# Kernel tuning notes

Measured on AMD Instinct MI355X. Metric: run time of the kernel, lower is better.

Reference implementation:

```python
import jax, jax.numpy as jnp
import numpy as np

# JAX reference for BERN-NN-Implicit LayerModule.forward.
# Semantics: for each output node i,
#   combined_over[i]  = sum_j relu(W)[i,j]*inputs_over[j] + (-relu(-W))[i,j]*inputs_under[j] + bias[i]
#   combined_under[i] = sum_j (-relu(-W))[i,j]*inputs_over[j] + relu(W)[i,j]*inputs_under[j] + bias[i]
# With all input Bernstein polynomials at equal degree, SumModule reduces to addition
# and prod_input_weights reduces to a weighted sum over the previous-layer neuron axis.

N_IN = 64      # previous-layer neurons
SIZE = 64      # nodes in this layer
G = 513        # Bernstein coefficient grid per dim (degree 512 + 1), dims = 2


def setup_inputs() -> dict:
    key = jax.random.key(0)
    k1, k2, k3, k4 = jax.random.split(key, 4)
    return {
        "inputs_under": jax.random.normal(k1, (N_IN, G, G), dtype=jnp.float32),
        "inputs_over": jax.random.normal(k2, (N_IN, G, G), dtype=jnp.float32),
        "weights": jax.random.normal(k3, (SIZE, N_IN), dtype=jnp.float32),
        "biases": jax.random.normal(k4, (SIZE,), dtype=jnp.float32),
        "layer_idx": 0,
    }


def reference(inputs_under, inputs_over, weights, biases, layer_idx):
    w_pos = jax.nn.relu(weights)          # [size, n_in]
    w_neg = -jax.nn.relu(-weights)        # [size, n_in]
    b = biases[:, None, None]             # [size, 1, 1]
    # [size, G, G] Bernstein coefficient grids per output node
    combined_over = (jnp.einsum("oi,ixy->oxy", w_pos, inputs_over)
                     + jnp.einsum("oi,ixy->oxy", w_neg, inputs_under)) + b
    combined_under = (jnp.einsum("oi,ixy->oxy", w_neg, inputs_over)
                      + jnp.einsum("oi,ixy->oxy", w_pos, inputs_under)) + b
    return combined_under, combined_over
```

## Files before the change

### kernel.cpp

```cpp
#include <hip/hip_runtime.h>

constexpr int PIX   = 513 * 513;
constexpr int NTILE = 128;

typedef short bf16x8 __attribute__((ext_vector_type(8)));
typedef float f32x4  __attribute__((ext_vector_type(4)));

__device__ __forceinline__ unsigned short f2bf(float f) {
    unsigned u = __builtin_bit_cast(unsigned, f);
    u += 0x7fffu + ((u >> 16) & 1u);
    return (unsigned short)(u >> 16);
}

__global__ __launch_bounds__(256, 2) void mfma_bounds_kernel(
    const float* __restrict__ under,
    const float* __restrict__ over,
    const float* __restrict__ W,
    const float* __restrict__ bias,
    float* __restrict__ out_under,
    float* __restrict__ out_over)
{
    __shared__ alignas(16) unsigned short Wl[128 * 128];
    __shared__ alignas(16) unsigned short Xt[NTILE * 128];
    __shared__ float Bl[64];

    const int t = threadIdx.x;
    const int pxbase = blockIdx.x * NTILE;

    if (pxbase + NTILE > PIX) {
        if (t < 128) {
            const int m = t;
            const int o = m & 63;
            const float* prim = (m < 64) ? over  : under;
            const float* sec  = (m < 64) ? under : over;
            for (int p = pxbase; p < PIX; ++p) {
                float acc = bias[o];
                for (int i = 0; i < 64; ++i) {
                    const float w = W[o * 64 + i];
                    acc += fmaxf(w, 0.f) * prim[(size_t)i * PIX + p]
                         + fminf(w, 0.f) * sec [(size_t)i * PIX + p];
                }
                if (m < 64) out_over [(size_t)m        * PIX + p] = acc;
                else        out_under[(size_t)(m - 64) * PIX + p] = acc;
            }
        }
        return;
    }

    #pragma unroll 4
    for (int e = 0; e < 32; ++e) {
        const int pidx = t + 256 * e;
        const int r  = pidx >> 6;
        const int c0 = (pidx & 63) * 2;
        const float w0 = W[(r & 63) * 64 + (c0 & 63)];
        const float w1 = W[(r & 63) * 64 + ((c0 + 1) & 63)];
        const bool same = ((c0 < 64) == (r < 64));
        const float v0 = same ? fmaxf(w0, 0.f) : fminf(w0, 0.f);
        const float v1 = same ? fmaxf(w1, 0.f) : fminf(w1, 0.f);
        const unsigned pack = (unsigned)f2bf(v0) | ((unsigned)f2bf(v1) << 16);
        const int off = r * 256 + ((c0 * 2) ^ ((r & 7) << 4));
        *(unsigned*)((char*)Wl + off) = pack;
    }
    if (t < 64) Bl[t] = bias[t];

    {
        const int px    = t & 127;
        const int khalf = t >> 7;
        const float* src = khalf ? under : over;
        const size_t p = (size_t)pxbase + px;
        #pragma unroll 8
        for (int j = 0; j < 32; ++j) {
            const int row = 2 * j;
            const float x0 = src[(size_t)row       * PIX + p];
            const float x1 = src[(size_t)(row + 1) * PIX + p];
            const unsigned pack = (unsigned)f2bf(x0) | ((unsigned)f2bf(x1) << 16);
            const int kbyte = 4 * j + 128 * khalf;
            const int off = px * 256 + (kbyte ^ ((px & 7) << 4));
            *(unsigned*)((char*)Xt + off) = pack;
        }
    }
    __syncthreads();

    const int wv   = t >> 6;
    const int lane = t & 63;
    const int lrow = lane & 15;
    const int lg   = lane >> 4;
    const int m0   = wv * 32;

    float bf[2][4];
    #pragma unroll
    for (int mt = 0; mt < 2; ++mt)
        #pragma unroll
        for (int r = 0; r < 4; ++r)
            bf[mt][r] = Bl[(m0 + mt * 16 + lg * 4 + r) & 63];

    bf16x8 A[2][4];
    #pragma unroll
    for (int mt = 0; mt < 2; ++mt)
        #pragma unroll
        for (int ks = 0; ks < 4; ++ks) {
            const int row = m0 + mt * 16 + lrow;
            const int ch  = ks * 4 + lg;
            A[mt][ks] = *(const bf16x8*)((const char*)Wl +
                          row * 256 + ((ch * 16) ^ ((row & 7) << 4)));
        }

    f32x4 acc[2][8];
    #pragma unroll
    for (int mt = 0; mt < 2; ++mt)
        #pragma unroll
        for (int nt = 0; nt < 8; ++nt) {
            f32x4 v = {bf[mt][0], bf[mt][1], bf[mt][2], bf[mt][3]};
            acc[mt][nt] = v;
        }

    #pragma unroll
    for (int nt = 0; nt < 8; ++nt) {
        bf16x8 Bf[4];
        #pragma unroll
        for (int ks = 0; ks < 4; ++ks) {
            const int prow = nt * 16 + lrow;
            const int ch   = ks * 4 + lg;
            Bf[ks] = *(const bf16x8*)((const char*)Xt +
                       prow * 256 + ((ch * 16) ^ ((prow & 7) << 4)));
        }
        #pragma unroll
        for (int mt = 0; mt < 2; ++mt)
            #pragma unroll
            for (int ks = 0; ks < 4; ++ks)
                acc[mt][nt] = __builtin_amdgcn_mfma_f32_16x16x32_bf16(
                    A[mt][ks], Bf[ks], acc[mt][nt], 0, 0, 0);
    }

    #pragma unroll
    for (int mt = 0; mt < 2; ++mt)
        #pragma unroll
        for (int r = 0; r < 4; ++r) {
            const int m = m0 + mt * 16 + lg * 4 + r;
            float* base = (m < 64) ? (out_over  + (size_t)m        * PIX)
                                   : (out_under + (size_t)(m - 64) * PIX);
            #pragma unroll
            for (int nt = 0; nt < 8; ++nt)
                __builtin_nontemporal_store(acc[mt][nt][r],
                    base + pxbase + nt * 16 + lrow);
        }
}

extern "C" void kernel_launch(void* const* d_in, const int* in_sizes, int n_in,
                              void* d_out, int out_size, void* d_ws, size_t ws_size,
                              hipStream_t stream) {
    const float* under = (const float*)d_in[0];
    const float* over  = (const float*)d_in[1];
    const float* W     = (const float*)d_in[2];
    const float* bias  = (const float*)d_in[3];
    float* out_under = (float*)d_out;
    float* out_over  = out_under + (size_t)64 * PIX;

    const int blocks = (PIX + NTILE - 1) / NTILE;
    mfma_bounds_kernel<<<blocks, 256, 0, stream>>>(under, over, W, bias,
                                                   out_under, out_over);
}
```

Measured before the change: 71.94 us.

## Load weights directly into registers, drop LDS weight tile, raise occupancy

```diff
diff --git a/kernel.cpp b/kernel.cpp
--- a/kernel.cpp
+++ b/kernel.cpp
@@ -11,8 +11,11 @@
     u += 0x7fffu + ((u >> 16) & 1u);
     return (unsigned short)(u >> 16);
 }
+__device__ __forceinline__ unsigned pack2(float a, float b) {
+    return (unsigned)f2bf(a) | ((unsigned)f2bf(b) << 16);
+}
 
-__global__ __launch_bounds__(256, 2) void mfma_bounds_kernel(
+__global__ __launch_bounds__(256, 4) void mfma_bounds_kernel(
     const float* __restrict__ under,
     const float* __restrict__ over,
     const float* __restrict__ W,
@@ -20,9 +23,7 @@
     float* __restrict__ out_under,
     float* __restrict__ out_over)
 {
-    __shared__ alignas(16) unsigned short Wl[128 * 128];
     __shared__ alignas(16) unsigned short Xt[NTILE * 128];
-    __shared__ float Bl[64];
 
     const int t = threadIdx.x;
     const int pxbase = blockIdx.x * NTILE;
@@ -47,39 +48,31 @@
         return;
     }
 
-    #pragma unroll 4
-    for (int e = 0; e < 32; ++e) {
-        const int pidx = t + 256 * e;
-        const int r  = pidx >> 6;
-        const int c0 = (pidx & 63) * 2;
-        const float w0 = W[(r & 63) * 64 + (c0 & 63)];
-        const float w1 = W[(r & 63) * 64 + ((c0 + 1) & 63)];
-        const bool same = ((c0 < 64) == (r < 64));
-        const float v0 = same ? fmaxf(w0, 0.f) : fminf(w0, 0.f);
-        const float v1 = same ? fmaxf(w1, 0.f) : fminf(w1, 0.f);
-        const unsigned pack = (unsigned)f2bf(v0) | ((unsigned)f2bf(v1) << 16);
-        const int off = r * 256 + ((c0 * 2) ^ ((r & 7) << 4));
-        *(unsigned*)((char*)Wl + off) = pack;
-    }
-    if (t < 64) Bl[t] = bias[t];
-
     {
         const int px    = t & 127;
         const int khalf = t >> 7;
         const float* src = khalf ? under : over;
-        const size_t p = (size_t)pxbase + px;
-        #pragma unroll 8
-        for (int j = 0; j < 32; ++j) {
-            const int row = 2 * j;
-            const float x0 = src[(size_t)row       * PIX + p];
-            const float x1 = src[(size_t)(row + 1) * PIX + p];
-            const unsigned pack = (unsigned)f2bf(x0) | ((unsigned)f2bf(x1) << 16);
-            const int kbyte = 4 * j + 128 * khalf;
-            const int off = px * 256 + (kbyte ^ ((px & 7) << 4));
-            *(unsigned*)((char*)Xt + off) = pack;
+        const size_t p  = (size_t)pxbase + px;
+        const int xw    = (px & 7) << 4;
+        #pragma unroll
+        for (int seg = 0; seg < 8; ++seg) {
+            float v0 = src[(size_t)(seg * 8 + 0) * PIX + p];
+            float v1 = src[(size_t)(seg * 8 + 1) * PIX + p];
+            float v2 = src[(size_t)(seg * 8 + 2) * PIX + p];
+            float v3 = src[(size_t)(seg * 8 + 3) * PIX + p];
+            float v4 = src[(size_t)(seg * 8 + 4) * PIX + p];
+            float v5 = src[(size_t)(seg * 8 + 5) * PIX + p];
+            float v6 = src[(size_t)(seg * 8 + 6) * PIX + p];
+            float v7 = src[(size_t)(seg * 8 + 7) * PIX + p];
+            int4 pk;
+            pk.x = (int)pack2(v0, v1);
+            pk.y = (int)pack2(v2, v3);
+            pk.z = (int)pack2(v4, v5);
+            pk.w = (int)pack2(v6, v7);
+            const int off = px * 256 + ((khalf * 128 + seg * 16) ^ xw);
+            *(int4*)((char*)Xt + off) = pk;
         }
     }
-    __syncthreads();
 
     const int wv   = t >> 6;
     const int lane = t & 63;
@@ -87,63 +80,84 @@
     const int lg   = lane >> 4;
     const int m0   = wv * 32;
 
-    float bf[2][4];
+    bf16x8 A[2][4];
+    #pragma unroll
+    for (int mt = 0; mt < 2; ++mt) {
+        const int m = m0 + mt * 16 + lrow;
+        const float* wr = W + (m & 63) * 64;
+        #pragma unroll
+        for (int ks = 0; ks < 4; ++ks) {
+            const int kbase = ks * 32 + lg * 8;
+            const bool same = ((kbase < 64) == (m < 64));
+            const float4 wa = *(const float4*)(wr + (kbase & 63));
+            const float4 wb = *(const float4*)(wr + (kbase & 63) + 4);
+            bf16x8 f;
+            f[0] = (short)f2bf(same ? fmaxf(wa.x, 0.f) : fminf(wa.x, 0.f));
+            f[1] = (short)f2bf(same ? fmaxf(wa.y, 0.f) : fminf(wa.y, 0.f));
+            f[2] = (short)f2bf(same ? fmaxf(wa.z, 0.f) : fminf(wa.z, 0.f));
+            f[3] = (short)f2bf(same ? fmaxf(wa.w, 0.f) : fminf(wa.w, 0.f));
+            f[4] = (short)f2bf(same ? fmaxf(wb.x, 0.f) : fminf(wb.x, 0.f));
+            f[5] = (short)f2bf(same ? fmaxf(wb.y, 0.f) : fminf(wb.y, 0.f));
+            f[6] = (short)f2bf(same ? fmaxf(wb.z, 0.f) : fminf(wb.z, 0.f));
+            f[7] = (short)f2bf(same ? fmaxf(wb.w, 0.f) : fminf(wb.w, 0.f));
+            A[mt][ks] = f;
+        }
+    }
+
+    float bb[2][4];
     #pragma unroll
     for (int mt = 0; mt < 2; ++mt)
         #pragma unroll
         for (int r = 0; r < 4; ++r)
-            bf[mt][r] = Bl[(m0 + mt * 16 + lg * 4 + r) & 63];
+            bb[mt][r] = bias[(m0 + mt * 16 + lg * 4 + r) & 63];
 
-    bf16x8 A[2][4];
-    #pragma unroll
-    for (int mt = 0; mt < 2; ++mt)
-        #pragma unroll
-        for (int ks = 0; ks < 4; ++ks) {
-            const int row = m0 + mt * 16 + lrow;
-            const int ch  = ks * 4 + lg;
-            A[mt][ks] = *(const bf16x8*)((const char*)Wl +
-                          row * 256 + ((ch * 16) ^ ((row & 7) << 4)));
-        }
+    __syncthreads();
 
-    f32x4 acc[2][8];
-    #pragma unroll
-    for (int mt = 0; mt < 2; ++mt)
-        #pragma unroll
-        for (int nt = 0; nt < 8; ++nt) {
-            f32x4 v = {bf[mt][0], bf[mt][1], bf[mt][2], bf[mt][3]};
-            acc[mt][nt] = v;
-        }
+    const int xwr = (lrow & 7) << 4;
 
     #pragma unroll
-    for (int nt = 0; nt < 8; ++nt) {
-        bf16x8 Bf[4];
-        #pragma unroll
-        for (int ks = 0; ks < 4; ++ks) {
-            const int prow = nt * 16 + lrow;
-            const int ch   = ks * 4 + lg;
-            Bf[ks] = *(const bf16x8*)((const char*)Xt +
-                       prow * 256 + ((ch * 16) ^ ((prow & 7) << 4)));
-        }
+    for (int h = 0; h < 2; ++h) {
+        f32x4 acc[2][4];
         #pragma unroll
         for (int mt = 0; mt < 2; ++mt)
             #pragma unroll
-            for (int ks = 0; ks < 4; ++ks)
-                acc[mt][nt] = __builtin_amdgcn_mfma_f32_16x16x32_bf16(
-                    A[mt][ks], Bf[ks], acc[mt][nt], 0, 0, 0);
+            for (int n4 = 0; n4 < 4; ++n4) {
+                f32x4 v = {bb[mt][0], bb[mt][1], bb[mt][2], bb[mt][3]};
+                acc[mt][n4] = v;
+            }
+
+        #pragma unroll
+        for (int n4 = 0; n4 < 4; ++n4) {
+            const int nt   = h * 4 + n4;
+            const int prow = nt * 16 + lrow;
+            bf16x8 Bf[4];
+            #pragma unroll
+            for (int ks = 0; ks < 4; ++ks) {
+                const int ch = ks * 4 + lg;
+                Bf[ks] = *(const bf16x8*)((const char*)Xt +
+                           prow * 256 + ((ch * 16) ^ xwr));
+            }
+            #pragma unroll
+            for (int mt = 0; mt < 2; ++mt)
+                #pragma unroll
+                for (int ks = 0; ks < 4; ++ks)
+                    acc[mt][n4] = __builtin_amdgcn_mfma_f32_16x16x32_bf16(
+                        A[mt][ks], Bf[ks], acc[mt][n4], 0, 0, 0);
+        }
+
+        #pragma unroll
+        for (int mt = 0; mt < 2; ++mt)
+            #pragma unroll
+            for (int r = 0; r < 4; ++r) {
+                const int m = m0 + mt * 16 + lg * 4 + r;
+                float* base = (m < 64) ? (out_over  + (size_t)m        * PIX)
+                                       : (out_under + (size_t)(m - 64) * PIX);
+                #pragma unroll
+                for (int n4 = 0; n4 < 4; ++n4)
+                    __builtin_nontemporal_store(acc[mt][n4][r],
+                        base + pxbase + (h * 4 + n4) * 16 + lrow);
+            }
     }
-
-    #pragma unroll
-    for (int mt = 0; mt < 2; ++mt)
-        #pragma unroll
-        for (int r = 0; r < 4; ++r) {
-            const int m = m0 + mt * 16 + lg * 4 + r;
-            float* base = (m < 64) ? (out_over  + (size_t)m        * PIX)
-                                   : (out_under + (size_t)(m - 64) * PIX);
-            #pragma unroll
-            for (int nt = 0; nt < 8; ++nt)
-                __builtin_nontemporal_store(acc[mt][nt][r],
-                    base + pxbase + nt * 16 + lrow);
-        }
 }
 
 extern "C" void kernel_launch(void* const* d_in, const int* in_sizes, int n_in,
```

Result: slower. 106.4 us (+47.8%).

## Precompute bf16 weight matrix in prep kernel and use 512-thread blocks

Applied to the files above, without the earlier changes.

```diff
diff --git a/kernel.cpp b/kernel.cpp
--- a/kernel.cpp
+++ b/kernel.cpp
@@ -6,13 +6,26 @@
 typedef short bf16x8 __attribute__((ext_vector_type(8)));
 typedef float f32x4  __attribute__((ext_vector_type(4)));
 
+__device__ unsigned short g_Wbig[128 * 128];
+
 __device__ __forceinline__ unsigned short f2bf(float f) {
     unsigned u = __builtin_bit_cast(unsigned, f);
     u += 0x7fffu + ((u >> 16) & 1u);
     return (unsigned short)(u >> 16);
 }
+__device__ __forceinline__ unsigned pack2(float a, float b) {
+    return (unsigned)f2bf(a) | ((unsigned)f2bf(b) << 16);
+}
 
-__global__ __launch_bounds__(256, 2) void mfma_bounds_kernel(
+__global__ __launch_bounds__(256) void prep_kernel(const float* __restrict__ W) {
+    const int idx = blockIdx.x * 256 + threadIdx.x;
+    const int m = idx >> 7, k = idx & 127;
+    const float w = W[(m & 63) * 64 + (k & 63)];
+    const bool same = ((m < 64) == (k < 64));
+    g_Wbig[idx] = f2bf(same ? fmaxf(w, 0.f) : fminf(w, 0.f));
+}
+
+__global__ __launch_bounds__(512, 4) void mfma_bounds_kernel(
     const float* __restrict__ under,
     const float* __restrict__ over,
     const float* __restrict__ W,
@@ -20,9 +33,7 @@
     float* __restrict__ out_under,
     float* __restrict__ out_over)
 {
-    __shared__ alignas(16) unsigned short Wl[128 * 128];
     __shared__ alignas(16) unsigned short Xt[NTILE * 128];
-    __shared__ float Bl[64];
 
     const int t = threadIdx.x;
     const int pxbase = blockIdx.x * NTILE;
@@ -47,103 +58,84 @@
         return;
     }
 
-    #pragma unroll 4
-    for (int e = 0; e < 32; ++e) {
-        const int pidx = t + 256 * e;
-        const int r  = pidx >> 6;
-        const int c0 = (pidx & 63) * 2;
-        const float w0 = W[(r & 63) * 64 + (c0 & 63)];
-        const float w1 = W[(r & 63) * 64 + ((c0 + 1) & 63)];
-        const bool same = ((c0 < 64) == (r < 64));
-        const float v0 = same ? fmaxf(w0, 0.f) : fminf(w0, 0.f);
-        const float v1 = same ? fmaxf(w1, 0.f) : fminf(w1, 0.f);
-        const unsigned pack = (unsigned)f2bf(v0) | ((unsigned)f2bf(v1) << 16);
-        const int off = r * 256 + ((c0 * 2) ^ ((r & 7) << 4));
-        *(unsigned*)((char*)Wl + off) = pack;
-    }
-    if (t < 64) Bl[t] = bias[t];
-
     {
-        const int px    = t & 127;
-        const int khalf = t >> 7;
-        const float* src = khalf ? under : over;
+        const int px = t & 127;
+        const int kq = t >> 7;
+        const float* src = (kq < 2) ? over : under;
+        const int rbase = (kq & 1) * 32;
         const size_t p = (size_t)pxbase + px;
-        #pragma unroll 8
-        for (int j = 0; j < 32; ++j) {
-            const int row = 2 * j;
-            const float x0 = src[(size_t)row       * PIX + p];
-            const float x1 = src[(size_t)(row + 1) * PIX + p];
-            const unsigned pack = (unsigned)f2bf(x0) | ((unsigned)f2bf(x1) << 16);
-            const int kbyte = 4 * j + 128 * khalf;
-            const int off = px * 256 + (kbyte ^ ((px & 7) << 4));
-            *(unsigned*)((char*)Xt + off) = pack;
+        const int xw = (px & 7) << 4;
+        #pragma unroll
+        for (int j = 0; j < 4; ++j) {
+            const int r0 = rbase + j * 8;
+            float v0 = src[(size_t)(r0 + 0) * PIX + p];
+            float v1 = src[(size_t)(r0 + 1) * PIX + p];
+            float v2 = src[(size_t)(r0 + 2) * PIX + p];
+            float v3 = src[(size_t)(r0 + 3) * PIX + p];
+            float v4 = src[(size_t)(r0 + 4) * PIX + p];
+            float v5 = src[(size_t)(r0 + 5) * PIX + p];
+            float v6 = src[(size_t)(r0 + 6) * PIX + p];
+            float v7 = src[(size_t)(r0 + 7) * PIX + p];
+            int4 pk;
+            pk.x = (int)pack2(v0, v1);
+            pk.y = (int)pack2(v2, v3);
+            pk.z = (int)pack2(v4, v5);
+            pk.w = (int)pack2(v6, v7);
+            const int off = px * 256 + ((kq * 64 + j * 16) ^ xw);
+            *(int4*)((char*)Xt + off) = pk;
         }
     }
-    __syncthreads();
 
     const int wv   = t >> 6;
     const int lane = t & 63;
     const int lrow = lane & 15;
     const int lg   = lane >> 4;
-    const int m0   = wv * 32;
+    const int m0   = wv * 16;
 
-    float bf[2][4];
+    bf16x8 A[4];
     #pragma unroll
-    for (int mt = 0; mt < 2; ++mt)
-        #pragma unroll
-        for (int r = 0; r < 4; ++r)
-            bf[mt][r] = Bl[(m0 + mt * 16 + lg * 4 + r) & 63];
+    for (int ks = 0; ks < 4; ++ks)
+        A[ks] = *(const bf16x8*)&g_Wbig[(m0 + lrow) * 128 + ks * 32 + lg * 8];
 
-    bf16x8 A[2][4];
+    float bb[4];
     #pragma unroll
-    for (int mt = 0; mt < 2; ++mt)
-        #pragma unroll
-        for (int ks = 0; ks < 4; ++ks) {
-            const int row = m0 + mt * 16 + lrow;
-            const int ch  = ks * 4 + lg;
-            A[mt][ks] = *(const bf16x8*)((const char*)Wl +
-                          row * 256 + ((ch * 16) ^ ((row & 7) << 4)));
-        }
+    for (int r = 0; r < 4; ++r)
+        bb[r] = bias[(m0 + lg * 4 + r) & 63];
 
-    f32x4 acc[2][8];
+    __syncthreads();
+
+    const int xwr = (lrow & 7) << 4;
+
+    f32x4 acc[8];
     #pragma unroll
-    for (int mt = 0; mt < 2; ++mt)
-        #pragma unroll
-        for (int nt = 0; nt < 8; ++nt) {
-            f32x4 v = {bf[mt][0], bf[mt][1], bf[mt][2], bf[mt][3]};
-            acc[mt][nt] = v;
-        }
+    for (int nt = 0; nt < 8; ++nt) {
+        f32x4 v = {bb[0], bb[1], bb[2], bb[3]};
+        acc[nt] = v;
+    }
 
     #pragma unroll
     for (int nt = 0; nt < 8; ++nt) {
+        const int prow = nt * 16 + lrow;
         bf16x8 Bf[4];
         #pragma unroll
         for (int ks = 0; ks < 4; ++ks) {
-            const int prow = nt * 16 + lrow;
-            const int ch   = ks * 4 + lg;
-            Bf[ks] = *(const bf16x8*)((const char*)Xt +
-                       prow * 256 + ((ch * 16) ^ ((prow & 7) << 4)));
+            const int ch = ks * 4 + lg;
+            Bf[ks] = *(const bf16x8*)((const char*)Xt + prow * 256 + ((ch * 16) ^ xwr));
         }
         #pragma unroll
-        for (int mt = 0; mt < 2; ++mt)
-            #pragma unroll
-            for (int ks = 0; ks < 4; ++ks)
-                acc[mt][nt] = __builtin_amdgcn_mfma_f32_16x16x32_bf16(
-                    A[mt][ks], Bf[ks], acc[mt][nt], 0, 0, 0);
+        for (int ks = 0; ks < 4; ++ks)
+            acc[nt] = __builtin_amdgcn_mfma_f32_16x16x32_bf16(A[ks], Bf[ks], acc[nt], 0, 0, 0);
     }
 
     #pragma unroll
-    for (int mt = 0; mt < 2; ++mt)
+    for (int r = 0; r < 4; ++r) {
+        const int m = m0 + lg * 4 + r;
+        float* base = (m < 64) ? (out_over  + (size_t)m        * PIX)
+                               : (out_under + (size_t)(m - 64) * PIX);
         #pragma unroll
-        for (int r = 0; r < 4; ++r) {
-            const int m = m0 + mt * 16 + lg * 4 + r;
-            float* base = (m < 64) ? (out_over  + (size_t)m        * PIX)
-                                   : (out_under + (size_t)(m - 64) * PIX);
-            #pragma unroll
-            for (int nt = 0; nt < 8; ++nt)
-                __builtin_nontemporal_store(acc[mt][nt][r],
-                    base + pxbase + nt * 16 + lrow);
-        }
+        for (int nt = 0; nt < 8; ++nt)
+            __builtin_nontemporal_store(acc[nt][r], base + pxbase + nt * 16 + lrow);
+    }
 }
 
 extern "C" void kernel_launch(void* const* d_in, const int* in_sizes, int n_in,
@@ -156,7 +148,9 @@
     float* out_under = (float*)d_out;
     float* out_over  = out_under + (size_t)64 * PIX;
 
+    prep_kernel<<<64, 256, 0, stream>>>(W);
+
     const int blocks = (PIX + NTILE - 1) / NTILE;
-    mfma_bounds_kernel<<<blocks, 256, 0, stream>>>(under, over, W, bias,
+    mfma_bounds_kernel<<<blocks, 512, 0, stream>>>(under, over, W, bias,
                                                    out_under, out_over);
 }
```

After: 80.86 us. 12.4% more time.
